# Performance work log

Hardware: AMD Instinct MI355X
Metric: run time of the kernel (lower is better)

The kernel has to match this reference:

```python
import jax, jax.numpy as jnp
import numpy as np


def log_g(x):
    # log of g(x) = x + 0.5 for x>=0, sigmoid(x) for x<0
    return jnp.where(x >= 0, jnp.log(jax.nn.relu(x) + 0.5), -jax.nn.softplus(-x))


def setup_inputs() -> dict:
    key = jax.random.key(0)
    k1, k2, k3 = jax.random.split(key, 3)
    bs, seq_len, d_in, H = 4, 4096, 1024, 1024
    scale = 1.0 / np.sqrt(d_in)  # keep pre-activations O(1) so exp() in log-space scan stays finite
    x = jax.random.normal(k1, (bs, seq_len, d_in), dtype=jnp.float32)
    h_0 = jnp.zeros((bs, 1, H), dtype=jnp.float32)
    Wz = jax.random.normal(k2, (H, d_in), dtype=jnp.float32) * scale
    bz = jnp.zeros((H,), dtype=jnp.float32)
    Wh = jax.random.normal(k3, (H, d_in), dtype=jnp.float32) * scale
    bh = jnp.zeros((H,), dtype=jnp.float32)
    return {"x": x, "h_0": h_0, "Wz": Wz, "bz": bz, "Wh": Wh, "bh": bh}


def reference(x, h_0, Wz, bz, Wh, bh):
    bs, seq_len, _ = x.shape
    # gate and candidate pre-activations (two GEMMs)
    k = jnp.einsum("bsd,hd->bsh", x, Wz) + bz          # [bs, S, H]
    log_coeff = -jax.nn.softplus(k)                     # log(1 - z)
    log_z = -jax.nn.softplus(-k)                        # log(z)
    log_tilde_h = log_g(jnp.einsum("bsd,hd->bsh", x, Wh) + bh)
    log_h_0 = log_g(h_0)                                # [bs, 1, H]
    log_value = jnp.concatenate([log_h_0, log_z + log_tilde_h], axis=1)  # [bs, S+1, H]
    # log-space parallel scan: h_t = (1-z_t) h_{t-1} + z_t h~_t
    a_star = jnp.pad(jnp.cumsum(log_coeff, axis=1), ((0, 0), (1, 0), (0, 0)))  # [bs, S+1, H]
    log_h0_plus_b_star = jax.lax.cumlogsumexp(log_value - a_star, axis=1)
    log_prefix = a_star + log_h0_plus_b_star
    return jnp.exp(log_prefix)[:, 1:]                   # [bs, S, H]
```

## Files before the change

kernel.cpp:

```cpp
#include <hip/hip_runtime.h>
#include <cstddef>
#include <cstdint>

#define BSZ   4
#define SEQ   4096
#define DIN   1024
#define HDIM  1024
#define MTOT  (BSZ * SEQ)
#define NELE  ((size_t)MTOT * HDIM)
#define NX    ((size_t)MTOT * DIN)
#define NW    ((size_t)HDIM * DIN)
#define NCH   128
#define CL    (SEQ / NCH)

#define X4 (NX / 4)
#define W4 (NW / 4)

#define GBM 256
#define GBN 128
#define GBK 64
#define NKT (DIN / GBK)

using bf16x8 = __attribute__((ext_vector_type(8))) __bf16;
using f32x4  = __attribute__((ext_vector_type(4))) float;

__device__ __forceinline__ float bf2f(unsigned int u16bits) {
    union { unsigned int i; float f; } v;
    v.i = u16bits << 16;
    return v.f;
}
__device__ __forceinline__ unsigned int pk2(float a, float b) {
    union { float f; unsigned int i; } ua, ub; ua.f = a; ub.f = b;
    return ((ua.i + 0x8000u) >> 16) | ((ub.i + 0x8000u) & 0xffff0000u);
}

__device__ __forceinline__ void gload16(const void* g, void* l) {
    __builtin_amdgcn_global_load_lds(
        (const __attribute__((address_space(1))) unsigned int*)g,
        (__attribute__((address_space(3))) unsigned int*)l, 16, 0, 0);
}

__global__ __launch_bounds__(256) void cvt_bf16(
    const float* __restrict__ x, const float* __restrict__ wz,
    const float* __restrict__ wh, unsigned short* __restrict__ xb,
    unsigned short* __restrict__ zb, unsigned short* __restrict__ hb)
{
    const size_t i = (size_t)blockIdx.x * 256 + threadIdx.x;
    const float4* s; uint4* d; size_t off;
    const size_t xh = X4 / 2, wh4 = W4 / 2;
    if (i < xh)            { s = (const float4*)x;  d = (uint4*)xb; off = i; }
    else if (i < xh + wh4) { s = (const float4*)wz; d = (uint4*)zb; off = i - xh; }
    else                   { s = (const float4*)wh; d = (uint4*)hb; off = i - xh - wh4; }
    const float4 v0 = s[2 * off];
    const float4 v1 = s[2 * off + 1];
    uint4 r;
    r.x = pk2(v0.x, v0.y); r.y = pk2(v0.z, v0.w);
    r.z = pk2(v1.x, v1.y); r.w = pk2(v1.z, v1.w);
    d[off] = r;
}

#define SBAR  __builtin_amdgcn_sched_barrier(0)
#define PRIO1 __builtin_amdgcn_s_setprio(1)
#define PRIO0 __builtin_amdgcn_s_setprio(0)

#define MFMA1(acc, va, vb) \
    acc = __builtin_amdgcn_mfma_f32_16x16x32_bf16(va, vb, acc, 0, 0, 0)

#define MFMA_PAIR(P, AV, S)                                                    \
    _Pragma("unroll")                                                          \
    for (int i_ = 0; i_ < 2; ++i_) {                                           \
        _Pragma("unroll")                                                      \
        for (int nt_ = 0; nt_ < 2; ++nt_) {                                    \
            MFMA1(accz[2*(P)+i_][nt_], AV[i_][0], Bz[S][nt_][0]);              \
            MFMA1(acch[2*(P)+i_][nt_], AV[i_][0], Bh[S][nt_][0]);              \
            MFMA1(accz[2*(P)+i_][nt_], AV[i_][1], Bz[S][nt_][1]);              \
            MFMA1(acch[2*(P)+i_][nt_], AV[i_][1], Bh[S][nt_][1]);              \
        }                                                                      \
    }

#define READ_A(AV, MTP, B)                                                     \
    AV[0][0] = *(const bf16x8*)((B) + aBase + (2*(MTP)+0)*2048 + k0o);         \
    AV[0][1] = *(const bf16x8*)((B) + aBase + (2*(MTP)+0)*2048 + k1o);         \
    AV[1][0] = *(const bf16x8*)((B) + aBase + (2*(MTP)+1)*2048 + k0o);         \
    AV[1][1] = *(const bf16x8*)((B) + aBase + (2*(MTP)+1)*2048 + k1o);

#define READ_B_HALF(SS, NT, B)                                                 \
    Bz[SS][NT][0] = *(const bf16x8*)((B) + zBase + (NT)*2048 + k0o);           \
    Bz[SS][NT][1] = *(const bf16x8*)((B) + zBase + (NT)*2048 + k1o);           \
    Bh[SS][NT][0] = *(const bf16x8*)((B) + hBase + (NT)*2048 + k0o);           \
    Bh[SS][NT][1] = *(const bf16x8*)((B) + hBase + (NT)*2048 + k1o);

#define STAGE8(BN, KO)                                                         \
    gload16(gA + (KO),          (BN) + ldsA);                                  \
    gload16(gA + (KO) + 16384,  (BN) + ldsA + 512);                            \
    gload16(gA + (KO) + 32768,  (BN) + ldsA + 1024);                           \
    gload16(gA + (KO) + 49152,  (BN) + ldsA + 1536);                           \
    gload16(gZ + (KO),          (BN) + ldsZ);                                  \
    gload16(gZ + (KO) + 16384,  (BN) + ldsZ + 512);                            \
    gload16(gH + (KO),          (BN) + ldsH);                                  \
    gload16(gH + (KO) + 16384,  (BN) + ldsH + 512);

#define TILE(KT, S)                                                            \
    {                                                                          \
        const int ktv = (KT);                                                  \
        const char*     bcc = (const char*)&smem[S][0];                        \
        unsigned short* bcw = &smem[S][0];                                     \
        const char*     bnc = (const char*)&smem[(S) ^ 1][0];                  \
        const bool pf = (ktv + 1 < NKT);                                       \
        const size_t ko2 = (size_t)(ktv + 2) * 128;                            \
                                                                       \
        READ_A(A1, 1, bcc)                                                     \
        PRIO1; MFMA_PAIR(0, A0, S) PRIO0; SBAR;                                \
                                                                       \
        READ_A(A0, 2, bcc)                                                     \
        PRIO1; MFMA_PAIR(1, A1, S) PRIO0; SBAR;                                \
              \
        READ_A(A1, 3, bcc)                                                     \
        asm volatile("s_waitcnt lgkmcnt(0)" ::: "memory");                     \
        SBAR;                                                                  \
        __builtin_amdgcn_s_barrier();                                          \
        if (ktv + 2 < NKT) { STAGE8(bcw, ko2) }                                \
        PRIO1; MFMA_PAIR(2, A0, S) PRIO0; SBAR;                                \
         \
        if (pf) {                                                              \
            if (ktv + 2 < NKT) { asm volatile("s_waitcnt vmcnt(8)" ::: "memory"); } \
            else               { asm volatile("s_waitcnt vmcnt(0)" ::: "memory"); } \
            __builtin_amdgcn_s_barrier();                                      \
            READ_B_HALF((S) ^ 1, 0, bnc)                                       \
            READ_A(A0, 0, bnc)                                                 \
        }                                                                      \
        PRIO1; MFMA_PAIR(3, A1, S) PRIO0; SBAR;                                \
        if (pf) { READ_B_HALF((S) ^ 1, 1, bnc) }                               \
    }

__global__ __launch_bounds__(512, 1) void gemm_act_8ph(
    const unsigned short* __restrict__ xb, const unsigned short* __restrict__ zb,
    const unsigned short* __restrict__ hb, const float* __restrict__ bz,
    const float* __restrict__ bh, unsigned int* __restrict__ ab,
    float* __restrict__ carryA, float* __restrict__ carryB)
{
    __shared__ unsigned short smem[2][32768];

    const int tid  = threadIdx.x;
    const int wid  = tid >> 6;
    const int lane = tid & 63;
    const int lm   = lane & 15;
    const int q    = lane >> 4;
    const int wr   = wid >> 2;
    const int wc   = wid & 3;

    const int bid = blockIdx.x;
    const int swz = (bid & 7) * 64 + (bid >> 3);
    const int ty  = swz >> 3;
    const int tx  = swz & 7;
    const int m0  = ty * GBM;
    const int n0  = tx * GBN;

    const int l8   = lane >> 3;
    const int sl   = lane & 7;
    const int scol = 16 * (sl ^ l8);
    const char* gA = (const char*)xb + ((size_t)(m0 + wid * 32 + l8) * DIN) * 2 + scol;
    const char* gZ = (const char*)zb + ((size_t)(n0 + wid * 16 + l8) * DIN) * 2 + scol;
    const char* gH = (const char*)hb + ((size_t)(n0 + wid * 16 + l8) * DIN) * 2 + scol;
    const int ldsA = wid * 2048;
    const int ldsZ = 16384 + wid * 1024;
    const int ldsH = 24576 + wid * 1024;

    const int sw  = (lm & 7) << 4;
    const int k0o = (q * 16) ^ sw;
    const int k1o = (64 + q * 16) ^ sw;
    const int aBase = (wr * 128 + lm) * 128;
    const int zBase = 32768 + (wc * 32 + lm) * 128;
    const int hBase = 49152 + (wc * 32 + lm) * 128;

    f32x4 accz[8][2], acch[8][2];
#pragma unroll
    for (int mt = 0; mt < 8; ++mt)
#pragma unroll
        for (int nt = 0; nt < 2; ++nt) {
            accz[mt][nt] = (f32x4){0.f, 0.f, 0.f, 0.f};
            acch[mt][nt] = (f32x4){0.f, 0.f, 0.f, 0.f};
        }

    bf16x8 A0[2][2], A1[2][2];
    bf16x8 Bz[2][2][2], Bh[2][2][2];

    {
        unsigned short* b0 = &smem[0][0];
        unsigned short* b1 = &smem[1][0];
        const char*     b0c = (const char*)b0;
        STAGE8(b0, 0)
        STAGE8(b1, 128)
        asm volatile("s_waitcnt vmcnt(8)" ::: "memory");
        __builtin_amdgcn_s_barrier();
        READ_B_HALF(0, 0, b0c)
        READ_B_HALF(0, 1, b0c)
        READ_A(A0, 0, b0c)
    }

    for (int kt = 0; kt < NKT; kt += 2) {
        TILE(kt, 0)
        TILE(kt + 1, 1)
    }

    const int bi  = m0 >> 12;
    const int cb0 = ((m0 & 4095) >> 5) + wr * 4;

#pragma unroll
    for (int nt = 0; nt < 2; ++nt) {
        const int col = n0 + wc * 32 + nt * 16 + lm;
        const float bzv = bz[col];
        const float bhv = bh[col];
#pragma unroll
        for (int pr = 0; pr < 4; ++pr) {
            float CA = 1.f, CB = 0.f;
#pragma unroll
            for (int mi = 0; mi < 2; ++mi) {
                const int mt   = pr * 2 + mi;
                const int row0 = m0 + wr * 128 + mt * 16 + q * 4;
                float A = 1.f, B = 0.f;
#pragma unroll
                for (int r = 0; r < 4; ++r) {
                    const float kpre = accz[mt][nt][r] + bzv;
                    const float hpre = acch[mt][nt][r] + bhv;
                    const float ez   = __expf(-kpre);
                    const float zv   = 1.0f / (1.0f + ez);
                    const float avv  = ez * zv;
                    const float g    = (hpre >= 0.f) ? (hpre + 0.5f)
                                                     : (1.0f / (1.0f + __expf(-hpre)));
                    const float bv   = zv * g;
                    ab[(size_t)(row0 + r) * HDIM + col] = pk2(avv, bv);
                    A = avv * A;
                    B = fmaf(avv, B, bv);
                }
                float A2 = __shfl_xor(A, 16, 64);
                float B2 = __shfl_xor(B, 16, 64);
                B = (q & 1) ? fmaf(A, B2, B) : fmaf(A2, B, B2);
                A = A * A2;
                A2 = __shfl_xor(A, 32, 64);
                B2 = __shfl_xor(B, 32, 64);
                B = (q & 2) ? fmaf(A, B2, B) : fmaf(A2, B, B2);
                A = A * A2;
                CB = fmaf(A, CB, B);
                CA = A * CA;
            }
            if (q == 0) {
                const int cseq = cb0 + pr;
                const size_t ci = ((size_t)(cseq * BSZ + bi)) * HDIM + col;
                carryA[ci] = CA;
                carryB[ci] = CB;
            }
        }
    }
}

__global__ __launch_bounds__(256) void scan_phaseB(
    const float* __restrict__ h0, const float* __restrict__ carryA,
    const float* __restrict__ carryB, float* __restrict__ hin)
{
    const int h  = blockIdx.x * 256 + threadIdx.x;
    const int bi = blockIdx.y;
    const float v = h0[(size_t)bi * HDIM + h];
    float hr = (v >= 0.0f) ? (v + 0.5f) : (1.0f / (1.0f + __expf(-v)));
    for (int c0 = 0; c0 < NCH; c0 += 8) {
        float a[8], b[8];
#pragma unroll
        for (int j = 0; j < 8; ++j) {
            const size_t ci = ((size_t)(c0 + j) * BSZ + bi) * HDIM + h;
            a[j] = carryA[ci];
            b[j] = carryB[ci];
        }
#pragma unroll
        for (int j = 0; j < 8; ++j) {
            const size_t ci = ((size_t)(c0 + j) * BSZ + bi) * HDIM + h;
            hin[ci] = hr;
            hr = fmaf(a[j], hr, b[j]);
        }
    }
}

__global__ __launch_bounds__(256) void scan_phaseC(
    const unsigned int* __restrict__ ab, const float* __restrict__ hin,
    float* __restrict__ out)
{
    const int c  = blockIdx.x;
    const int bi = blockIdx.y;
    const int h  = threadIdx.x * 4;
    size_t idx = ((size_t)bi * SEQ + (size_t)c * CL) * HDIM + h;
    const size_t ci = ((size_t)c * BSZ + bi) * HDIM + h;
    float4 hr = *(const float4*)&hin[ci];
#pragma unroll 4
    for (int t = 0; t < CL; ++t) {
        const uint4 v = *(const uint4*)&ab[idx];
        hr.x = fmaf(bf2f(v.x & 0xffffu), hr.x, bf2f(v.x >> 16));
        hr.y = fmaf(bf2f(v.y & 0xffffu), hr.y, bf2f(v.y >> 16));
        hr.z = fmaf(bf2f(v.z & 0xffffu), hr.z, bf2f(v.z >> 16));
        hr.w = fmaf(bf2f(v.w & 0xffffu), hr.w, bf2f(v.w >> 16));
        *(float4*)&out[idx] = hr;
        idx += HDIM;
    }
}

extern "C" void kernel_launch(void* const* d_in, const int* in_sizes, int n_in,
                              void* d_out, int out_size, void* d_ws, size_t ws_size,
                              hipStream_t stream)
{
    const float* x  = (const float*)d_in[0];
    const float* h0 = (const float*)d_in[1];
    const float* Wz = (const float*)d_in[2];
    const float* bz = (const float*)d_in[3];
    const float* Wh = (const float*)d_in[4];
    const float* bh = (const float*)d_in[5];
    float* out = (float*)d_out;

    unsigned int*   ab  = (unsigned int*)d_ws;
    unsigned short* xbf = (unsigned short*)(ab + NELE);
    unsigned short* zbf = xbf + NX;
    unsigned short* hbf = zbf + NW;
    float* carryA = (float*)(hbf + NW);
    float* carryB = carryA + (size_t)NCH * BSZ * HDIM;
    float* hin    = carryB + (size_t)NCH * BSZ * HDIM;

    const int cvtBlocks = (int)((X4 + 2 * W4) / 2 / 256);
    cvt_bf16<<<cvtBlocks, 256, 0, stream>>>(x, Wz, Wh, xbf, zbf, hbf);

    dim3 gGrid((MTOT / GBM) * (HDIM / GBN));
    gemm_act_8ph<<<gGrid, 512, 0, stream>>>(xbf, zbf, hbf, bz, bh, ab, carryA, carryB);

    dim3 bGrid(HDIM / 256, BSZ);
    scan_phaseB<<<bGrid, 256, 0, stream>>>(h0, carryA, carryB, hin);

    dim3 cGrid(NCH, BSZ);
    scan_phaseC<<<cGrid, 256, 0, stream>>>(ab, hin, out);
}
```

Baseline: 241.3 us.

## Shallow GEMM prefetch to one stage, narrow convert and scan per-thread work

The GEMM staging loads the next K tile at the start of each iteration into the other buffer and waits for all loads, instead of keeping two tiles in flight with partial waits. The bf16 conversion kernel handles one float4 per thread over twice the blocks. The chunk scan kernel processes two columns per thread across a doubled grid and prefetches the next timestep's coefficients. This trades GEMM load latency hiding for simpler synchronisation and raises parallelism in the elementwise kernels.

```diff
diff --git a/kernel.cpp b/kernel.cpp
--- a/kernel.cpp
+++ b/kernel.cpp
@@ -46,16 +46,14 @@
     unsigned short* __restrict__ zb, unsigned short* __restrict__ hb)
 {
     const size_t i = (size_t)blockIdx.x * 256 + threadIdx.x;
-    const float4* s; uint4* d; size_t off;
-    const size_t xh = X4 / 2, wh4 = W4 / 2;
-    if (i < xh)            { s = (const float4*)x;  d = (uint4*)xb; off = i; }
-    else if (i < xh + wh4) { s = (const float4*)wz; d = (uint4*)zb; off = i - xh; }
-    else                   { s = (const float4*)wh; d = (uint4*)hb; off = i - xh - wh4; }
-    const float4 v0 = s[2 * off];
-    const float4 v1 = s[2 * off + 1];
-    uint4 r;
-    r.x = pk2(v0.x, v0.y); r.y = pk2(v0.z, v0.w);
-    r.z = pk2(v1.x, v1.y); r.w = pk2(v1.z, v1.w);
+    const float4* s; uint2* d; size_t off;
+    if (i < X4)           { s = (const float4*)x;  d = (uint2*)xb; off = i; }
+    else if (i < X4 + W4) { s = (const float4*)wz; d = (uint2*)zb; off = i - X4; }
+    else                  { s = (const float4*)wh; d = (uint2*)hb; off = i - X4 - W4; }
+    const float4 v = s[off];
+    uint2 r;
+    r.x = pk2(v.x, v.y);
+    r.y = pk2(v.z, v.w);
     d[off] = r;
 }
 
@@ -104,27 +102,23 @@
     {                                                                          \
         const int ktv = (KT);                                                  \
         const char*     bcc = (const char*)&smem[S][0];                        \
-        unsigned short* bcw = &smem[S][0];                                     \
-        const char*     bnc = (const char*)&smem[(S) ^ 1][0];                  \
+        unsigned short* bn  = &smem[(S) ^ 1][0];                               \
+        const char*     bnc = (const char*)bn;                                 \
         const bool pf = (ktv + 1 < NKT);                                       \
-        const size_t ko2 = (size_t)(ktv + 2) * 128;                            \
+        const size_t ko = (size_t)(ktv + 1) * 128;                             \
                                                                        \
+        if (pf) { STAGE8(bn, ko) }                                             \
         READ_A(A1, 1, bcc)                                                     \
         PRIO1; MFMA_PAIR(0, A0, S) PRIO0; SBAR;                                \
                                                                        \
         READ_A(A0, 2, bcc)                                                     \
         PRIO1; MFMA_PAIR(1, A1, S) PRIO0; SBAR;                                \
-              \
+                                                                       \
         READ_A(A1, 3, bcc)                                                     \
-        asm volatile("s_waitcnt lgkmcnt(0)" ::: "memory");                     \
-        SBAR;                                                                  \
-        __builtin_amdgcn_s_barrier();                                          \
-        if (ktv + 2 < NKT) { STAGE8(bcw, ko2) }                                \
         PRIO1; MFMA_PAIR(2, A0, S) PRIO0; SBAR;                                \
-         \
+                \
         if (pf) {                                                              \
-            if (ktv + 2 < NKT) { asm volatile("s_waitcnt vmcnt(8)" ::: "memory"); } \
-            else               { asm volatile("s_waitcnt vmcnt(0)" ::: "memory"); } \
+            asm volatile("s_waitcnt vmcnt(0)" ::: "memory");                   \
             __builtin_amdgcn_s_barrier();                                      \
             READ_B_HALF((S) ^ 1, 0, bnc)                                       \
             READ_A(A0, 0, bnc)                                                 \
@@ -187,11 +181,9 @@
 
     {
         unsigned short* b0 = &smem[0][0];
-        unsigned short* b1 = &smem[1][0];
         const char*     b0c = (const char*)b0;
         STAGE8(b0, 0)
-        STAGE8(b1, 128)
-        asm volatile("s_waitcnt vmcnt(8)" ::: "memory");
+        asm volatile("s_waitcnt vmcnt(0)" ::: "memory");
         __builtin_amdgcn_s_barrier();
         READ_B_HALF(0, 0, b0c)
         READ_B_HALF(0, 1, b0c)
@@ -285,18 +277,19 @@
 {
     const int c  = blockIdx.x;
     const int bi = blockIdx.y;
-    const int h  = threadIdx.x * 4;
+    const int h  = (blockIdx.z * 256 + threadIdx.x) * 2;
     size_t idx = ((size_t)bi * SEQ + (size_t)c * CL) * HDIM + h;
     const size_t ci = ((size_t)c * BSZ + bi) * HDIM + h;
-    float4 hr = *(const float4*)&hin[ci];
+    float2 hr = *(const float2*)&hin[ci];
+    uint2 v = *(const uint2*)&ab[idx];
 #pragma unroll 4
     for (int t = 0; t < CL; ++t) {
-        const uint4 v = *(const uint4*)&ab[idx];
+        uint2 vn;
+        if (t + 1 < CL) vn = *(const uint2*)&ab[idx + HDIM];
         hr.x = fmaf(bf2f(v.x & 0xffffu), hr.x, bf2f(v.x >> 16));
         hr.y = fmaf(bf2f(v.y & 0xffffu), hr.y, bf2f(v.y >> 16));
-        hr.z = fmaf(bf2f(v.z & 0xffffu), hr.z, bf2f(v.z >> 16));
-        hr.w = fmaf(bf2f(v.w & 0xffffu), hr.w, bf2f(v.w >> 16));
-        *(float4*)&out[idx] = hr;
+        *(float2*)&out[idx] = hr;
+        v = vn;
         idx += HDIM;
     }
 }
@@ -321,7 +314,7 @@
     float* carryB = carryA + (size_t)NCH * BSZ * HDIM;
     float* hin    = carryB + (size_t)NCH * BSZ * HDIM;
 
-    const int cvtBlocks = (int)((X4 + 2 * W4) / 2 / 256);
+    const int cvtBlocks = (int)((X4 + 2 * W4) / 256);
     cvt_bf16<<<cvtBlocks, 256, 0, stream>>>(x, Wz, Wh, xbf, zbf, hbf);
 
     dim3 gGrid((MTOT / GBM) * (HDIM / GBN));
@@ -330,6 +323,6 @@
     dim3 bGrid(HDIM / 256, BSZ);
     scan_phaseB<<<bGrid, 256, 0, stream>>>(h0, carryA, carryB, hin);
 
-    dim3 cGrid(NCH, BSZ);
+    dim3 cGrid(NCH, BSZ, 2);
     scan_phaseC<<<cGrid, 256, 0, stream>>>(ab, hin, out);
 }
```

After: 231.3 us. -4.1%, faster.
